# Optimization experiments

Hardware: AMD Instinct MI355X
Metric: run time of the kernel (lower is better)

Reference implementation:

```python
import jax, jax.numpy as jnp
import numpy as np

N_LEVELS = 16
N_FEATS = 2
LOG2_T = 19
BASE_RES = 16.0
FINEST_RES = 512.0
N_POINTS = 1048576

# (8,3) corner offsets, i outer, then j, then k (matches BOX_OFFSETS ordering)
_OFFSETS = np.array([[i, j, k] for i in (0, 1) for j in (0, 1) for k in (0, 1)], dtype=np.uint32)
# Teschner spatial-hash primes for 3D; uint32 so multiplication wraps mod 2^32 like int32 torch
_PRIMES = np.array([1, 2654435761, 805459861], dtype=np.uint32)


def setup_inputs() -> dict:
    key = jax.random.key(0)
    k1, k2 = jax.random.split(key)
    x = jax.random.uniform(k1, (N_POINTS, 3), dtype=jnp.float32)  # points inside [0,1]^3 bbox
    # per-level hash tables, init U(-1e-4, 1e-4) as in the module
    tables = jax.random.uniform(k2, (N_LEVELS, 1 << LOG2_T, N_FEATS),
                                dtype=jnp.float32, minval=-1e-4, maxval=1e-4)
    return {"x": x, "tables": tables}


def _encode(x, tables):
    box_min = jnp.zeros((3,), dtype=x.dtype)
    box_max = jnp.ones((3,), dtype=x.dtype)
    hash_mask = jnp.uint32((1 << LOG2_T) - 1)

    b = jnp.exp((jnp.log(FINEST_RES) - jnp.log(BASE_RES)) / (N_LEVELS - 1))
    res = jnp.floor(BASE_RES * b ** jnp.arange(N_LEVELS, dtype=x.dtype))  # (L,)

    keep_mask = jnp.all((x >= box_min) & (x <= box_max), axis=-1)  # (N,)
    xc = jnp.clip(x, box_min, box_max)

    grid = (box_max - box_min) / res[:, None]                # (L,3) voxel size per level
    rel = xc[:, None, :] - box_min                           # (N,L,3) via broadcast
    bl_f = jnp.floor(rel / grid)                             # (N,L,3) bottom-left voxel index
    vmin = bl_f * grid + box_min                             # (N,L,3)
    w = (xc[:, None, :] - vmin) / grid                       # (N,L,3) trilinear weights

    # 8 corner integer coords, hashed
    bl = bl_f.astype(jnp.uint32)                             # (N,L,3)
    corners = bl[:, :, None, :] + jnp.asarray(_OFFSETS)      # (N,L,8,3)
    prod = corners * jnp.asarray(_PRIMES)                    # wraps mod 2^32
    hashed = (prod[..., 0] ^ prod[..., 1] ^ prod[..., 2]) & hash_mask  # (N,L,8)

    # gather each level's corners from its own table: tables (L,T,F), hashed (N,L,8)
    emb = jax.vmap(lambda tab, ix: tab[ix], in_axes=(0, 1), out_axes=1)(tables, hashed)  # (N,L,8,F)

    wx = w[..., 0:1]  # (N,L,1)
    wy = w[..., 1:2]
    wz = w[..., 2:3]
    c00 = emb[..., 0, :] * (1 - wx) + emb[..., 4, :] * wx
    c01 = emb[..., 1, :] * (1 - wx) + emb[..., 5, :] * wx
    c10 = emb[..., 2, :] * (1 - wx) + emb[..., 6, :] * wx
    c11 = emb[..., 3, :] * (1 - wx) + emb[..., 7, :] * wx
    c0 = c00 * (1 - wy) + c10 * wy
    c1 = c01 * (1 - wy) + c11 * wy
    c = c0 * (1 - wz) + c1 * wz                              # (N,L,F)

    out = c.reshape(x.shape[0], N_LEVELS * N_FEATS)          # concat over levels
    return out, keep_mask


def reference(x, tables):
    return _encode(x, tables)
```

## Files before the change

### kernel.cpp

```cpp
#include <hip/hip_runtime.h>
#include <stdint.h>

typedef float f2 __attribute__((ext_vector_type(2)));
typedef float f4 __attribute__((ext_vector_type(4)));

__constant__ float c_res[16] = {16.f, 20.f, 25.f, 32.f, 40.f, 50.f, 64.f, 80.f,
                                101.f, 128.f, 161.f, 203.f, 256.f, 322.f, 406.f, 512.f};

#define HASH_MASK ((1u << 19) - 1u)
#define P1 2654435761u
#define P2 805459861u
#define PTS_PER_THREAD 4

template <bool WRITE_TMP>
__global__ __launch_bounds__(256, 4) void hash_encode_kernel(
    const float* __restrict__ x,
    const float* __restrict__ tables,
    f2* __restrict__ tmp,
    float* __restrict__ out,
    float* __restrict__ mask_out,
    int n_points,
    int blocks_per_phase,
    int level_base_arg,
    int two_phase)
{
    int bid = blockIdx.x;
    int level_base = level_base_arg;
    if (two_phase) {
        level_base = 0;
        if (bid >= blocks_per_phase) { bid -= blocks_per_phase; level_base = 8; }
    }
    int level = (bid & 7) + level_base;
    int trow = two_phase ? level : (bid & 7);
    int chunk = bid >> 3;

    float res  = c_res[level];
    float grid = 1.0f / res;
    const f2* __restrict__ tab =
        (const f2*)tables + ((size_t)level << 19);
    const f4* __restrict__ tab4 = (const f4*)tab;

    int pbase = chunk * (256 * PTS_PER_THREAD) + threadIdx.x;

    uint32_t idx[PTS_PER_THREAD][8];
    float wx[PTS_PER_THREAD], wy[PTS_PER_THREAD], wz[PTS_PER_THREAD];
    bool valid[PTS_PER_THREAD];
    bool bxodd[PTS_PER_THREAD];
    int pp[PTS_PER_THREAD];

    #pragma unroll
    for (int s = 0; s < PTS_PER_THREAD; ++s) {
        int p = pbase + s * 256;
        pp[s] = p;
        valid[s] = (p < n_points);
        int pc = valid[s] ? p : 0;

        float x0 = x[3 * (size_t)pc + 0];
        float x1 = x[3 * (size_t)pc + 1];
        float x2 = x[3 * (size_t)pc + 2];

        if (level == 0 && valid[s]) {
            bool keep = (x0 >= 0.f) & (x0 <= 1.f) &
                        (x1 >= 0.f) & (x1 <= 1.f) &
                        (x2 >= 0.f) & (x2 <= 1.f);
            mask_out[pc] = keep ? 1.0f : 0.0f;
        }

        x0 = fminf(fmaxf(x0, 0.f), 1.f);
        x1 = fminf(fmaxf(x1, 0.f), 1.f);
        x2 = fminf(fmaxf(x2, 0.f), 1.f);

        float b0 = floorf(x0 / grid);
        float b1 = floorf(x1 / grid);
        float b2 = floorf(x2 / grid);

        wx[s] = (x0 - b0 * grid) / grid;
        wy[s] = (x1 - b1 * grid) / grid;
        wz[s] = (x2 - b2 * grid) / grid;

        uint32_t bx = (uint32_t)b0;
        uint32_t by = (uint32_t)b1;
        uint32_t bz = (uint32_t)b2;

        bxodd[s] = (bx & 1u) != 0u;

        uint32_t hx0 = bx;        uint32_t hx1 = bx + 1u;
        uint32_t hy0 = by * P1;   uint32_t hy1 = hy0 + P1;
        uint32_t hz0 = bz * P2;   uint32_t hz1 = hz0 + P2;

        idx[s][0] = (hx0 ^ hy0 ^ hz0) & HASH_MASK;
        idx[s][1] = (hx0 ^ hy0 ^ hz1) & HASH_MASK;
        idx[s][2] = (hx0 ^ hy1 ^ hz0) & HASH_MASK;
        idx[s][3] = (hx0 ^ hy1 ^ hz1) & HASH_MASK;
        idx[s][4] = (hx1 ^ hy0 ^ hz0) & HASH_MASK;
        idx[s][5] = (hx1 ^ hy0 ^ hz1) & HASH_MASK;
        idx[s][6] = (hx1 ^ hy1 ^ hz0) & HASH_MASK;
        idx[s][7] = (hx1 ^ hy1 ^ hz1) & HASH_MASK;
    }

    f2 e[PTS_PER_THREAD][8];
    #pragma unroll
    for (int s = 0; s < PTS_PER_THREAD; ++s) {
        if (!bxodd[s]) {
            #pragma unroll
            for (int j = 0; j < 4; ++j) {
                uint32_t q = idx[s][j];
                f4 v = tab4[q >> 1];
                f2 lov = {v.x, v.y};
                f2 hiv = {v.z, v.w};
                bool hi = (q & 1u) != 0u;
                e[s][j]     = hi ? hiv : lov;
                e[s][j + 4] = hi ? lov : hiv;
            }
        } else {
            #pragma unroll
            for (int c = 0; c < 8; ++c)
                e[s][c] = tab[idx[s][c]];
        }
    }

    #pragma unroll
    for (int s = 0; s < PTS_PER_THREAD; ++s) {
        float owx = 1.f - wx[s], owy = 1.f - wy[s], owz = 1.f - wz[s];

        f2 c00 = e[s][0] * owx + e[s][4] * wx[s];
        f2 c01 = e[s][1] * owx + e[s][5] * wx[s];
        f2 c10 = e[s][2] * owx + e[s][6] * wx[s];
        f2 c11 = e[s][3] * owx + e[s][7] * wx[s];

        f2 c0 = c00 * owy + c10 * wy[s];
        f2 c1 = c01 * owy + c11 * wy[s];

        f2 cv = c0 * owz + c1 * wz[s];

        if (valid[s]) {
            if constexpr (WRITE_TMP) {
                tmp[(size_t)trow * n_points + pp[s]] = cv;
            } else {
                f2* dst = (f2*)(out + (size_t)pp[s] * 32) + level;
                *dst = cv;
            }
        }
    }
}

template <int NL>
__global__ __launch_bounds__(256) void transpose_kernel(
    const f2* __restrict__ tmp,
    float* __restrict__ out,
    int n_points,
    int lb)
{
    __shared__ f2 lds[NL][257];
    const int FP = NL / 2;
    int t = threadIdx.x;
    int p0 = blockIdx.x * 256;

    #pragma unroll
    for (int l = 0; l < NL; ++l) {
        int p = p0 + t;
        lds[l][t] = tmp[(size_t)l * n_points + (p < n_points ? p : 0)];
    }
    __syncthreads();

    f4* out4 = (f4*)out;
    #pragma unroll
    for (int i = 0; i < FP; ++i) {
        int g = i * 256 + t;
        int pidx = g / FP;
        int k = g % FP;
        f2 a = lds[2 * k][pidx];
        f2 b = lds[2 * k + 1][pidx];
        f4 w = {a.x, a.y, b.x, b.y};
        int p = p0 + pidx;
        if (p < n_points)
            out4[(size_t)p * 8 + lb / 2 + k] = w;
    }
}

extern "C" void kernel_launch(void* const* d_in, const int* in_sizes, int n_in,
                              void* d_out, int out_size, void* d_ws, size_t ws_size,
                              hipStream_t stream) {
    const float* x      = (const float*)d_in[0];
    const float* tables = (const float*)d_in[1];
    float* out = (float*)d_out;
    int n_points = in_sizes[0] / 3;
    float* mask_out = out + (size_t)n_points * 32;

    int chunks = (n_points + 256 * PTS_PER_THREAD - 1) / (256 * PTS_PER_THREAD);
    int blocks_per_phase = chunks * 8;
    int tblocks = (n_points + 255) / 256;

    size_t need_full = (size_t)n_points * 16 * sizeof(f2);
    size_t need_half = (size_t)n_points * 8 * sizeof(f2);

    if (n_points > 0 && ws_size >= need_full) {
        f2* tmp = (f2*)d_ws;
        hipLaunchKernelGGL((hash_encode_kernel<true>), dim3(blocks_per_phase * 2),
                           dim3(256), 0, stream,
                           x, tables, tmp, out, mask_out, n_points,
                           blocks_per_phase, 0, 1);
        hipLaunchKernelGGL((transpose_kernel<16>), dim3(tblocks), dim3(256), 0,
                           stream, tmp, out, n_points, 0);
    } else if (n_points > 0 && ws_size >= need_half) {
        f2* tmp = (f2*)d_ws;
        hipLaunchKernelGGL((hash_encode_kernel<true>), dim3(blocks_per_phase),
                           dim3(256), 0, stream,
                           x, tables, tmp, out, mask_out, n_points,
                           blocks_per_phase, 0, 0);
        hipLaunchKernelGGL((transpose_kernel<8>), dim3(tblocks), dim3(256), 0,
                           stream, tmp, out, n_points, 0);
        hipLaunchKernelGGL((hash_encode_kernel<true>), dim3(blocks_per_phase),
                           dim3(256), 0, stream,
                           x, tables, tmp, out, mask_out, n_points,
                           blocks_per_phase, 8, 0);
        hipLaunchKernelGGL((transpose_kernel<8>), dim3(tblocks), dim3(256), 0,
                           stream, tmp, out, n_points, 8);
    } else {
        hipLaunchKernelGGL((hash_encode_kernel<false>), dim3(blocks_per_phase * 2),
                           dim3(256), 0, stream,
                           x, tables, (f2*)nullptr, out, mask_out, n_points,
                           blocks_per_phase, 0, 1);
    }
}
```

Baseline: 624.5 us.

## Overlap level 0-7 transpose with level 8-15 encoding in fused kernel

Result: slower. 676.0 us (+8.3%).

```diff
diff --git a/kernel.cpp b/kernel.cpp
--- a/kernel.cpp
+++ b/kernel.cpp
@@ -12,28 +12,16 @@
 #define P2 805459861u
 #define PTS_PER_THREAD 4
 
+
 template <bool WRITE_TMP>
-__global__ __launch_bounds__(256, 4) void hash_encode_kernel(
+__device__ __forceinline__ void encode_block(
     const float* __restrict__ x,
     const float* __restrict__ tables,
     f2* __restrict__ tmp,
     float* __restrict__ out,
     float* __restrict__ mask_out,
-    int n_points,
-    int blocks_per_phase,
-    int level_base_arg,
-    int two_phase)
-{
-    int bid = blockIdx.x;
-    int level_base = level_base_arg;
-    if (two_phase) {
-        level_base = 0;
-        if (bid >= blocks_per_phase) { bid -= blocks_per_phase; level_base = 8; }
-    }
-    int level = (bid & 7) + level_base;
-    int trow = two_phase ? level : (bid & 7);
-    int chunk = bid >> 3;
-
+    int n_points, int level, int trow, int chunk)
+{
     float res  = c_res[level];
     float grid = 1.0f / res;
     const f2* __restrict__ tab =
@@ -135,7 +123,8 @@
 
         if (valid[s]) {
             if constexpr (WRITE_TMP) {
-                tmp[(size_t)trow * n_points + pp[s]] = cv;
+                __builtin_nontemporal_store(cv,
+                    &tmp[(size_t)trow * n_points + pp[s]]);
             } else {
                 f2* dst = (f2*)(out + (size_t)pp[s] * 32) + level;
                 *dst = cv;
@@ -144,38 +133,114 @@
     }
 }
 
+__global__ __launch_bounds__(256, 4) void fused_kernel(
+    const float* __restrict__ x,
+    const float* __restrict__ tables,
+    f2* __restrict__ tmp,
+    float* __restrict__ out,
+    float* __restrict__ mask_out,
+    int n_points,
+    int n_tiles,
+    int tr_cnt,
+    int tr_row_base,
+    int tr_out_lb,
+    int enc_level_base,
+    int enc_trow_base)
+{
+    int g = (int)blockIdx.x >> 3;
+    int r = (int)blockIdx.x & 7;
+
+    if (tr_cnt > 0 && (g % 5) == 4) {
+        __shared__ f2 lds[8][257];
+        int tid = (g / 5) * 8 + r;
+        int trb = tr_cnt * 8;
+        int t = threadIdx.x;
+        f4* out4 = (f4*)out;
+        for (int tile = tid; tile < n_tiles; tile += trb) {
+            int p0 = tile * 256;
+            #pragma unroll
+            for (int l = 0; l < 8; ++l) {
+                int p = p0 + t;
+                lds[l][t] = tmp[(size_t)(tr_row_base + l) * n_points +
+                                (p < n_points ? p : 0)];
+            }
+            __syncthreads();
+            #pragma unroll
+            for (int i = 0; i < 4; ++i) {
+                int gi = i * 256 + t;
+                int pidx = gi >> 2;
+                int k = gi & 3;
+                f2 a = lds[2 * k][pidx];
+                f2 b = lds[2 * k + 1][pidx];
+                int p = p0 + pidx;
+                if (p < n_points) {
+                    f4 w = {a.x, a.y, b.x, b.y};
+                    out4[(size_t)p * 8 + tr_out_lb / 2 + k] = w;
+                }
+            }
+            __syncthreads();
+        }
+        return;
+    }
+
+    int gg = (tr_cnt > 0) ? (g - (g + 1) / 5) : g;
+    int level = r + enc_level_base;
+    int trow = r + enc_trow_base;
+    encode_block<true>(x, tables, tmp, out, mask_out, n_points,
+                       level, trow, gg);
+}
+
 template <int NL>
 __global__ __launch_bounds__(256) void transpose_kernel(
     const f2* __restrict__ tmp,
     float* __restrict__ out,
+    int n_points, int row_base, int out_lb, int n_tiles)
+{
+    __shared__ f2 lds[NL][257];
+    constexpr int FP = NL / 2;
+    int t = threadIdx.x;
+    f4* out4 = (f4*)out;
+    for (int tile = blockIdx.x; tile < n_tiles; tile += gridDim.x) {
+        int p0 = tile * 256;
+        #pragma unroll
+        for (int l = 0; l < NL; ++l) {
+            int p = p0 + t;
+            lds[l][t] = tmp[(size_t)(row_base + l) * n_points +
+                            (p < n_points ? p : 0)];
+        }
+        __syncthreads();
+        #pragma unroll
+        for (int i = 0; i < FP; ++i) {
+            int gi = i * 256 + t;
+            int pidx = gi / FP;
+            int k = gi % FP;
+            f2 a = lds[2 * k][pidx];
+            f2 b = lds[2 * k + 1][pidx];
+            int p = p0 + pidx;
+            if (p < n_points) {
+                f4 w = {a.x, a.y, b.x, b.y};
+                out4[(size_t)p * 8 + out_lb / 2 + k] = w;
+            }
+        }
+        __syncthreads();
+    }
+}
+
+__global__ __launch_bounds__(256, 4) void encode_direct_kernel(
+    const float* __restrict__ x,
+    const float* __restrict__ tables,
+    float* __restrict__ out,
+    float* __restrict__ mask_out,
     int n_points,
-    int lb)
-{
-    __shared__ f2 lds[NL][257];
-    const int FP = NL / 2;
-    int t = threadIdx.x;
-    int p0 = blockIdx.x * 256;
-
-    #pragma unroll
-    for (int l = 0; l < NL; ++l) {
-        int p = p0 + t;
-        lds[l][t] = tmp[(size_t)l * n_points + (p < n_points ? p : 0)];
-    }
-    __syncthreads();
-
-    f4* out4 = (f4*)out;
-    #pragma unroll
-    for (int i = 0; i < FP; ++i) {
-        int g = i * 256 + t;
-        int pidx = g / FP;
-        int k = g % FP;
-        f2 a = lds[2 * k][pidx];
-        f2 b = lds[2 * k + 1][pidx];
-        f4 w = {a.x, a.y, b.x, b.y};
-        int p = p0 + pidx;
-        if (p < n_points)
-            out4[(size_t)p * 8 + lb / 2 + k] = w;
-    }
+    int blocks_per_phase)
+{
+    int bid = blockIdx.x;
+    int level_base = 0;
+    if (bid >= blocks_per_phase) { bid -= blocks_per_phase; level_base = 8; }
+    int level = (bid & 7) + level_base;
+    int chunk = bid >> 3;
+    encode_block<false>(x, tables, nullptr, out, mask_out, n_points,
+                        level, level, chunk);
 }
 
 extern "C" void kernel_launch(void* const* d_in, const int* in_sizes, int n_in,
@@ -188,38 +253,43 @@
     float* mask_out = out + (size_t)n_points * 32;
 
     int chunks = (n_points + 256 * PTS_PER_THREAD - 1) / (256 * PTS_PER_THREAD);
-    int blocks_per_phase = chunks * 8;
-    int tblocks = (n_points + 255) / 256;
+    int n_tiles = (n_points + 255) / 256;
+    int tr_grid = n_tiles < 2048 ? n_tiles : 2048;
+    if (tr_grid < 1) tr_grid = 1;
 
     size_t need_full = (size_t)n_points * 16 * sizeof(f2);
     size_t need_half = (size_t)n_points * 8 * sizeof(f2);
 
     if (n_points > 0 && ws_size >= need_full) {
         f2* tmp = (f2*)d_ws;
-        hipLaunchKernelGGL((hash_encode_kernel<true>), dim3(blocks_per_phase * 2),
-                           dim3(256), 0, stream,
-                           x, tables, tmp, out, mask_out, n_points,
-                           blocks_per_phase, 0, 1);
-        hipLaunchKernelGGL((transpose_kernel<16>), dim3(tblocks), dim3(256), 0,
-                           stream, tmp, out, n_points, 0);
+        hipLaunchKernelGGL(fused_kernel, dim3(chunks * 8), dim3(256), 0, stream,
+                           x, tables, tmp, out, mask_out, n_points,
+                           n_tiles, 0, 0, 0, 0, 0);
+        int total = chunks + (chunks + 3) / 4;
+        if (total < 5) total = 5;
+        while (total - total / 5 < chunks) ++total;
+        int tr_cnt = total / 5;
+        hipLaunchKernelGGL(fused_kernel, dim3(total * 8), dim3(256), 0, stream,
+                           x, tables, tmp, out, mask_out, n_points,
+                           n_tiles, tr_cnt, 0, 0,
+                           8, 8);
+        hipLaunchKernelGGL((transpose_kernel<8>), dim3(tr_grid), dim3(256), 0,
+                           stream, tmp, out, n_points, 8, 8, n_tiles);
     } else if (n_points > 0 && ws_size >= need_half) {
         f2* tmp = (f2*)d_ws;
-        hipLaunchKernelGGL((hash_encode_kernel<true>), dim3(blocks_per_phase),
-                           dim3(256), 0, stream,
-                           x, tables, tmp, out, mask_out, n_points,
-                           blocks_per_phase, 0, 0);
-        hipLaunchKernelGGL((transpose_kernel<8>), dim3(tblocks), dim3(256), 0,
-                           stream, tmp, out, n_points, 0);
-        hipLaunchKernelGGL((hash_encode_kernel<true>), dim3(blocks_per_phase),
-                           dim3(256), 0, stream,
-                           x, tables, tmp, out, mask_out, n_points,
-                           blocks_per_phase, 8, 0);
-        hipLaunchKernelGGL((transpose_kernel<8>), dim3(tblocks), dim3(256), 0,
-                           stream, tmp, out, n_points, 8);
+        hipLaunchKernelGGL(fused_kernel, dim3(chunks * 8), dim3(256), 0, stream,
+                           x, tables, tmp, out, mask_out, n_points,
+                           n_tiles, 0, 0, 0, 0, 0);
+        hipLaunchKernelGGL((transpose_kernel<8>), dim3(tr_grid), dim3(256), 0,
+                           stream, tmp, out, n_points, 0, 0, n_tiles);
+        hipLaunchKernelGGL(fused_kernel, dim3(chunks * 8), dim3(256), 0, stream,
+                           x, tables, tmp, out, mask_out, n_points,
+                           n_tiles, 0, 0, 0, 8, 0);
+        hipLaunchKernelGGL((transpose_kernel<8>), dim3(tr_grid), dim3(256), 0,
+                           stream, tmp, out, n_points, 0, 8, n_tiles);
     } else {
-        hipLaunchKernelGGL((hash_encode_kernel<false>), dim3(blocks_per_phase * 2),
-                           dim3(256), 0, stream,
-                           x, tables, (f2*)nullptr, out, mask_out, n_points,
-                           blocks_per_phase, 0, 1);
-    }
-}
+        hipLaunchKernelGGL(encode_direct_kernel, dim3(chunks * 16), dim3(256),
+                           0, stream, x, tables, out, mask_out, n_points,
+                           chunks * 8);
+    }
+}
```
